# Kernel tuning notes

Measured on AMD Instinct MI355X. Metric: run time of the kernel, lower is better.

The kernel has to match this reference:

```python
import jax, jax.numpy as jnp
import numpy as np

NUM_EXPERTS = 8
TOP_K = 2
TOKENS = 4096
HIDDEN = 1024
INTER = 2048
INIT_STD = 0.01  # nnx.initializers.normal() default stddev


def setup_inputs() -> dict:
    key = jax.random.key(0)
    k1, k2, k3, k4, k5 = jax.random.split(key, 5)
    return {
        "inputs": jax.random.normal(k1, (TOKENS, HIDDEN), jnp.float32),
        "router_logits": jax.random.normal(k2, (TOKENS, NUM_EXPERTS), jnp.float32),
        "wi_0": jax.random.normal(k3, (NUM_EXPERTS, HIDDEN, INTER), jnp.float32) * INIT_STD,
        "wi_1": jax.random.normal(k4, (NUM_EXPERTS, HIDDEN, INTER), jnp.float32) * INIT_STD,
        "wo": jax.random.normal(k5, (NUM_EXPERTS, INTER, HIDDEN), jnp.float32) * INIT_STD,
    }


def reference(inputs, router_logits, wi_0, wi_1, wo):
    T, H = inputs.shape
    # --- top-k routing ---
    top_k_logits, top_k_indices = jax.lax.top_k(router_logits, TOP_K)  # [T, k]
    w = jax.nn.softmax(top_k_logits, axis=-1)
    w = w / jnp.sum(w, axis=-1, keepdims=True)  # (redundant renorm, kept faithful)
    # --- permute: sort token-expert pairs by expert id ---
    flat_experts = top_k_indices.reshape(-1)          # [T*k]
    sort_idx = jnp.argsort(flat_experts)              # stable sort -> token order within group
    token_idx = sort_idx // TOP_K                     # source token of each sorted slot
    x = inputs[token_idx]                             # [T*k, H] gathered/permuted tokens
    group_sizes = jnp.bincount(flat_experts, length=NUM_EXPERTS).astype(jnp.int32)
    # --- grouped (ragged) GEMM experts: silu(x@wi_0) * (x@wi_1) @ wo ---
    h0 = jax.lax.ragged_dot(x, wi_0, group_sizes, preferred_element_type=jnp.float32)
    h1 = jax.lax.ragged_dot(x, wi_1, group_sizes, preferred_element_type=jnp.float32)
    act = jax.nn.silu(h0) * h1                        # [T*k, INTER]
    y = jax.lax.ragged_dot(act, wo, group_sizes, preferred_element_type=jnp.float32)  # [T*k, H]
    # --- unpermute + weighted combine over top-k ---
    unsort = jnp.argsort(sort_idx)
    y = y[unsort].reshape(T, TOP_K, H)
    return jnp.sum(y * w[..., None], axis=1)          # [T, H]
```

## Files before the change

### kernel.cpp

```cpp
#include <hip/hip_runtime.h>
#include <hip/hip_bf16.h>

#define T_TOKENS 4096
#define HID 1024
#define INTER 2048
#define NEXP 8
#define TOPK 2
#define RTOT (T_TOKENS * TOPK)
#define BMT 128
#define BN 128
#define MAXT (RTOT / BMT + NEXP)

typedef __attribute__((ext_vector_type(8))) short bf16x8;
typedef __attribute__((ext_vector_type(4))) float f32x4;

typedef __attribute__((address_space(1))) const unsigned int gu32;
typedef __attribute__((address_space(3))) unsigned int lu32;

__device__ __forceinline__ void gl16(const void* g, void* l) {
  __builtin_amdgcn_global_load_lds((gu32*)g, (lu32*)l, 16, 0, 0);
}

__device__ __forceinline__ unsigned f2bf(float f) {
  union { float f; unsigned u; } v; v.f = f;
  unsigned u = v.u;
  return (u + 0x7FFFu + ((u >> 16) & 1u)) >> 16;
}

__device__ __forceinline__ float bf2f(unsigned short s) {
  union { unsigned u; float f; } v; v.u = ((unsigned)s) << 16;
  return v.f;
}

__device__ __forceinline__ int swz(int row, int kb) {
  return row * 128 + (kb ^ ((row & 7) << 4));
}

__device__ __forceinline__ void phase_barrier() {
  asm volatile("" ::: "memory");
  __builtin_amdgcn_s_barrier();
  asm volatile("" ::: "memory");
}

__device__ __forceinline__ int psig(int kap) { return kap ^ ((kap & 1) << 2); }

__global__ __launch_bounds__(1024)
void k_routing(const float* __restrict__ logits, int* ntiles,
               int* te2, int* tr02, int* tcnt2,
               float* pw, int* rows, float* rw, int* slotOf) {
  __shared__ int cnt[NEXP];
  __shared__ int cur[NEXP];
  const int tid = threadIdx.x;
  if (tid < NEXP) cnt[tid] = 0;
  __syncthreads();
#pragma unroll
  for (int j = 0; j < 4; ++j) {
    int t = j * 1024 + tid;
    float l[NEXP];
#pragma unroll
    for (int i = 0; i < NEXP; ++i) l[i] = logits[t * NEXP + i];
    int i0 = 0; float b0 = l[0];
#pragma unroll
    for (int i = 1; i < NEXP; ++i) if (l[i] > b0) { b0 = l[i]; i0 = i; }
    int i1 = -1; float b1 = -1e30f;
#pragma unroll
    for (int i = 0; i < NEXP; ++i) if (i != i0 && l[i] > b1) { b1 = l[i]; i1 = i; }
    float e = __expf(b1 - b0);
    float w0 = 1.f / (1.f + e);
    float w1 = e / (1.f + e);
    pw[2 * t] = w0; pw[2 * t + 1] = w1;
#pragma unroll
    for (int ex = 0; ex < NEXP; ++ex) {
      int c = __popcll(__ballot(i0 == ex)) + __popcll(__ballot(i1 == ex));
      if ((tid & 63) == 0 && c) atomicAdd(&cnt[ex], c);
    }
  }
  __syncthreads();
  if (tid == 0) {
    int off = 0, nm = 0;
    for (int e = 0; e < NEXP; ++e) {
      int c = cnt[e];
      cur[e] = off;
      for (int m0 = 0; m0 < c; m0 += BMT) {
        te2[nm] = e; tr02[nm] = off + m0; tcnt2[nm] = min(BMT, c - m0); ++nm;
      }
      off += c;
    }
    ntiles[1] = nm;
  }
  __syncthreads();
#pragma unroll
  for (int j = 0; j < 4; ++j) {
    int t = j * 1024 + tid;
    float l[NEXP];
#pragma unroll
    for (int i = 0; i < NEXP; ++i) l[i] = logits[t * NEXP + i];
    int i0 = 0; float b0 = l[0];
#pragma unroll
    for (int i = 1; i < NEXP; ++i) if (l[i] > b0) { b0 = l[i]; i0 = i; }
    int i1 = -1; float b1 = -1e30f;
#pragma unroll
    for (int i = 0; i < NEXP; ++i) if (i != i0 && l[i] > b1) { b1 = l[i]; i1 = i; }
    float e = __expf(b1 - b0);
    float ww[2] = {1.f / (1.f + e), e / (1.f + e)};
    int ee[2] = {i0, i1};
#pragma unroll
    for (int k = 0; k < TOPK; ++k) {
      int s = atomicAdd(&cur[ee[k]], 1);
      rows[s] = t;
      rw[s] = ww[k];
      slotOf[2 * t + k] = s;
    }
  }
}

__global__ __launch_bounds__(256)
void k_prep1r(const float* __restrict__ X, unsigned short* __restrict__ Xb,
              const float* __restrict__ W0, const float* __restrict__ W1,
              unsigned short* __restrict__ T0, unsigned short* __restrict__ T1,
              const float* __restrict__ logits, int* ntiles,
              int* te2, int* tr02, int* tcnt2,
              float* pw, int* rows, float* rw, int* slotOf) {
  int bid = blockIdx.x;
  const int tid = threadIdx.x;

  if (bid == 0) {
    __shared__ int cnt[NEXP];
    __shared__ int cur[NEXP];
    if (tid < NEXP) cnt[tid] = 0;
    __syncthreads();
#pragma unroll
    for (int j = 0; j < 16; ++j) {
      int t = j * 256 + tid;
      float l[NEXP];
#pragma unroll
      for (int i = 0; i < NEXP; ++i) l[i] = logits[t * NEXP + i];
      int i0 = 0; float b0 = l[0];
#pragma unroll
      for (int i = 1; i < NEXP; ++i) if (l[i] > b0) { b0 = l[i]; i0 = i; }
      int i1 = -1; float b1 = -1e30f;
#pragma unroll
      for (int i = 0; i < NEXP; ++i) if (i != i0 && l[i] > b1) { b1 = l[i]; i1 = i; }
      float e = __expf(b1 - b0);
      float w0 = 1.f / (1.f + e);
      pw[2 * t] = w0; pw[2 * t + 1] = 1.f - w0;
#pragma unroll
      for (int ex = 0; ex < NEXP; ++ex) {
        int c = __popcll(__ballot(i0 == ex)) + __popcll(__ballot(i1 == ex));
        if ((tid & 63) == 0 && c) atomicAdd(&cnt[ex], c);
      }
    }
    __syncthreads();
    if (tid == 0) {
      int off = 0, nm = 0;
      for (int e = 0; e < NEXP; ++e) {
        int c = cnt[e];
        cur[e] = off;
        for (int m0 = 0; m0 < c; m0 += BMT) {
          te2[nm] = e; tr02[nm] = off + m0; tcnt2[nm] = min(BMT, c - m0); ++nm;
        }
        off += c;
      }
      ntiles[1] = nm;
    }
    __syncthreads();
#pragma unroll
    for (int j = 0; j < 16; ++j) {
      int t = j * 256 + tid;
      float l[NEXP];
#pragma unroll
      for (int i = 0; i < NEXP; ++i) l[i] = logits[t * NEXP + i];
      int i0 = 0; float b0 = l[0];
#pragma unroll
      for (int i = 1; i < NEXP; ++i) if (l[i] > b0) { b0 = l[i]; i0 = i; }
      int i1 = -1; float b1 = -1e30f;
#pragma unroll
      for (int i = 0; i < NEXP; ++i) if (i != i0 && l[i] > b1) { b1 = l[i]; i1 = i; }
      float e = __expf(b1 - b0);
      float ww0 = 1.f / (1.f + e);
      int ee[2] = {i0, i1};
      float ww[2] = {ww0, 1.f - ww0};
#pragma unroll
      for (int k = 0; k < TOPK; ++k) {
        int s = atomicAdd(&cur[ee[k]], 1);
        rows[s] = t;
        rw[s] = ww[k];
        slotOf[2 * t + k] = s;
      }
    }
    return;
  }

  if (bid < 1025) {
    int base = (bid - 1) * 1024 + tid;
#pragma unroll
    for (int j = 0; j < 4; ++j) {
      int i = base + j * 256;
      float4 v = *(const float4*)(X + (size_t)i * 4);
      uint2 p;
      p.x = f2bf(v.x) | (f2bf(v.y) << 16);
      p.y = f2bf(v.z) | (f2bf(v.w) << 16);
      *(uint2*)(Xb + (size_t)i * 4) = p;
    }
    return;
  }
  bid -= 1025;
  const int w = bid >> 11;
  const int r = bid & 2047;
  const float* W = (w == 0) ? W0 : W1;
  unsigned short* T = (w == 0) ? T0 : T1;
  const int nt = r & 15, kt = (r >> 4) & 15, e = r >> 8;
  __shared__ float ls[64 * 128];
  const float* src = W + (size_t)e * HID * INTER + (size_t)(kt * 64) * INTER + nt * 128;
#pragma unroll
  for (int t = 0; t < 8; ++t) {
    int u = t * 256 + tid;
    int k = u >> 5, n4 = u & 31;
    float4 v = *(const float4*)(src + (size_t)k * INTER + n4 * 4);
    *(float4*)(ls + k * 128 + ((n4 ^ psig(k >> 3)) << 2)) = v;
  }
  __syncthreads();
  unsigned short* dst = T + (((size_t)e * 16 + nt) * 16 + kt) * 8192;
#pragma unroll
  for (int t = 0; t < 4; ++t) {
    int v = t * 256 + tid;
    int kt2 = v >> 9, n = (v >> 2) & 127, sw = v & 3;
    int kc = kt2 * 4 + (sw ^ ((n >> 1) & 3));
    const float* col = ls + (size_t)(kc * 8) * 128 +
                       (((n >> 2) ^ psig(kc)) << 2) + (n & 3);
    unsigned b[8];
#pragma unroll
    for (int i = 0; i < 8; ++i) b[i] = f2bf(col[i * 128]);
    uint4 q;
    q.x = b[0] | (b[1] << 16); q.y = b[2] | (b[3] << 16);
    q.z = b[4] | (b[5] << 16); q.w = b[6] | (b[7] << 16);
    *(uint4*)(dst + (size_t)v * 8) = q;
  }
}

__global__ __launch_bounds__(512, 4)
void k_gemm1w(const unsigned short* __restrict__ Xb,
              const unsigned short* __restrict__ WT0,
              const unsigned short* __restrict__ WT1,
              const float* __restrict__ WO,
              unsigned short* __restrict__ WTo,
              const int* __restrict__ ntiles, const int* __restrict__ te2,
              const int* __restrict__ tr02, const int* __restrict__ tcnt2,
              const int* __restrict__ rows,
              unsigned short* __restrict__ act) {
  const int ty = blockIdx.y;
  const int nt = blockIdx.x;
  const int tid = threadIdx.x;
  __shared__ __align__(16) unsigned char sm[49152];

  if (ty >= MAXT) {
    const int r = (ty - MAXT) * 16 + nt;
    const int ntt = r & 7, kt = (r >> 3) & 31, e = r >> 8;
    float* ls = (float*)sm;
    const float* src = WO + (size_t)e * INTER * HID + (size_t)(kt * 64) * HID + ntt * 128;
#pragma unroll
    for (int t = 0; t < 4; ++t) {
      int u = t * 512 + tid;
      int k = u >> 5, n4 = u & 31;
      float4 v = *(const float4*)(src + (size_t)k * HID + n4 * 4);
      *(float4*)(ls + k * 128 + ((n4 ^ psig(k >> 3)) << 2)) = v;
    }
    __syncthreads();
    unsigned short* dst = WTo + (((size_t)e * 8 + ntt) * 32 + kt) * 8192;
#pragma unroll
    for (int t = 0; t < 2; ++t) {
      int v = t * 512 + tid;
      int kt2 = v >> 9, n = (v >> 2) & 127, sw = v & 3;
      int kc = kt2 * 4 + (sw ^ ((n >> 1) & 3));
      const float* col = ls + (size_t)(kc * 8) * 128 +
                         (((n >> 2) ^ psig(kc)) << 2) + (n & 3);
      unsigned b[8];
#pragma unroll
      for (int i = 0; i < 8; ++i) b[i] = f2bf(col[i * 128]);
      uint4 q;
      q.x = b[0] | (b[1] << 16); q.y = b[2] | (b[3] << 16);
      q.z = b[4] | (b[5] << 16); q.w = b[6] | (b[7] << 16);
      *(uint4*)(dst + (size_t)v * 8) = q;
    }
    return;
  }

  if (ty >= ntiles[1]) return;
  const int e = te2[ty], row0 = tr02[ty], mcnt = tcnt2[ty];
  const int n0 = nt * BN;
  const int lane = tid & 63, wv = tid >> 6;
  const int mh = wv >> 2, nq = wv & 3;
  const int l15 = lane & 15, sl = lane >> 4;

  const int am = tid >> 2;
  const int atok = rows[row0 + (am < mcnt ? am : mcnt - 1)];
  const int askc = ((tid & 3) ^ ((tid >> 3) & 3)) * 8;
  const unsigned short* B0t = WT0 + ((size_t)e * 16 + nt) * 32 * 4096;
  const unsigned short* B1t = WT1 + ((size_t)e * 16 + nt) * 32 * 4096;

  int aoff[4], boff[2];
#pragma unroll
  for (int f = 0; f < 4; ++f) {
    int m = mh * 64 + f * 16 + l15;
    aoff[f] = m * 64 + ((sl ^ ((m >> 1) & 3)) << 4);
  }
#pragma unroll
  for (int g = 0; g < 2; ++g) {
    int n = nq * 32 + g * 16 + l15;
    boff[g] = n * 64 + ((sl ^ ((n >> 1) & 3)) << 4);
  }

  f32x4 acc0[4][2], acc1[4][2];
  const f32x4 zz = {0.f, 0.f, 0.f, 0.f};
#pragma unroll
  for (int f = 0; f < 4; ++f)
#pragma unroll
    for (int g = 0; g < 2; ++g) { acc0[f][g] = zz; acc1[f][g] = zz; }

  const int NT_K = HID / 32;

  gl16(Xb + (size_t)atok * HID + askc, sm + tid * 16);
  gl16(B0t + (size_t)tid * 8, sm + 8192 + tid * 16);
  gl16(B1t + (size_t)tid * 8, sm + 16384 + tid * 16);

  for (int t = 0; t < NT_K; ++t) {
    unsigned char* cur = sm + (t & 1) * 24576;
    unsigned char* nxt = sm + ((t + 1) & 1) * 24576;
    const int tn = (t + 1 < NT_K) ? (t + 1) : (NT_K - 1);

    gl16(Xb + (size_t)atok * HID + tn * 32 + askc, nxt + tid * 16);
    gl16(B0t + (size_t)tn * 4096 + tid * 8, nxt + 8192 + tid * 16);
    gl16(B1t + (size_t)tn * 4096 + tid * 8, nxt + 16384 + tid * 16);
    asm volatile("s_waitcnt vmcnt(3)" ::: "memory");
    __builtin_amdgcn_sched_barrier(0);
    phase_barrier();

    bf16x8 aA[4], b0q[2], b1q[2];
#pragma unroll
    for (int g = 0; g < 2; ++g) {
      b0q[g] = *(const bf16x8*)(cur + 8192 + boff[g]);
      b1q[g] = *(const bf16x8*)(cur + 16384 + boff[g]);
    }
#pragma unroll
    for (int f = 0; f < 4; ++f) aA[f] = *(const bf16x8*)(cur + aoff[f]);
    __builtin_amdgcn_s_setprio(1);
#pragma unroll
    for (int f = 0; f < 4; ++f)
#pragma unroll
      for (int g = 0; g < 2; ++g) {
        acc0[f][g] = __builtin_amdgcn_mfma_f32_16x16x32_bf16(aA[f], b0q[g], acc0[f][g], 0, 0, 0);
        acc1[f][g] = __builtin_amdgcn_mfma_f32_16x16x32_bf16(aA[f], b1q[g], acc1[f][g], 0, 0, 0);
      }
    __builtin_amdgcn_s_setprio(0);
    phase_barrier();
  }

#pragma unroll
  for (int f = 0; f < 4; ++f) {
#pragma unroll
    for (int r = 0; r < 4; ++r) {
      int m = mh * 64 + f * 16 + sl * 4 + r;
      if (m >= mcnt) continue;
      size_t base = (size_t)(row0 + m) * INTER + n0 + nq * 32 + l15;
#pragma unroll
      for (int g = 0; g < 2; ++g) {
        float h0 = acc0[f][g][r];
        float h1 = acc1[f][g][r];
        float s = h0 / (1.f + __expf(-h0));
        act[base + g * 16] = (unsigned short)f2bf(s * h1);
      }
    }
  }
}

__global__ __launch_bounds__(256, 4)
void k_gemm2n(const unsigned short* __restrict__ act,
              const unsigned short* __restrict__ WTo,
              const int* __restrict__ ntiles, const int* __restrict__ te2,
              const int* __restrict__ tr02, const int* __restrict__ tcnt2,
              unsigned short* __restrict__ y) {
  const int ty = blockIdx.y;
  if (ty >= ntiles[1]) return;
  const int e = te2[ty], row0 = tr02[ty], mcnt = tcnt2[ty];
  const int nt = blockIdx.x, n0 = nt * BN;
  const int tid = threadIdx.x, lane = tid & 63, wv = tid >> 6;
  const int wr = wv >> 1, wc = wv & 1;
  const int l15 = lane & 15, sl = lane >> 4;

  __shared__ __align__(16) unsigned char sm[32768];

  const int am0 = tid >> 2, am1 = 64 + (tid >> 2);
  const int ar0 = row0 + (am0 < mcnt ? am0 : mcnt - 1);
  const int ar1 = row0 + (am1 < mcnt ? am1 : mcnt - 1);
  const int askc = ((tid & 3) ^ ((tid >> 3) & 3)) * 8;
  const unsigned short* Bt = WTo + ((size_t)e * 8 + nt) * 64 * 4096;

  int aoff[4], boff[4];
#pragma unroll
  for (int f = 0; f < 4; ++f) {
    int m = wr * 64 + f * 16 + l15;
    aoff[f] = m * 64 + ((sl ^ ((m >> 1) & 3)) << 4);
    int n = wc * 64 + f * 16 + l15;
    boff[f] = n * 64 + ((sl ^ ((n >> 1) & 3)) << 4);
  }

  f32x4 acc[4][4];
  const f32x4 zz = {0.f, 0.f, 0.f, 0.f};
#pragma unroll
  for (int i = 0; i < 4; ++i)
#pragma unroll
    for (int j = 0; j < 4; ++j) acc[i][j] = zz;

  const int NT_K = INTER / 32;

  gl16(act + (size_t)ar0 * INTER + askc, sm + tid * 16);
  gl16(act + (size_t)ar1 * INTER + askc, sm + (256 + tid) * 16);
  gl16(Bt + (size_t)tid * 8, sm + 8192 + tid * 16);
  gl16(Bt + (size_t)(256 + tid) * 8, sm + 8192 + (256 + tid) * 16);

  for (int t = 0; t < NT_K; ++t) {
    unsigned char* cur = sm + (t & 1) * 16384;
    unsigned char* nxt = sm + ((t + 1) & 1) * 16384;
    const int tn = (t + 1 < NT_K) ? (t + 1) : (NT_K - 1);

    gl16(act + (size_t)ar0 * INTER + tn * 32 + askc, nxt + tid * 16);
    gl16(act + (size_t)ar1 * INTER + tn * 32 + askc, nxt + (256 + tid) * 16);
    gl16(Bt + (size_t)tn * 4096 + tid * 8, nxt + 8192 + tid * 16);
    gl16(Bt + ((size_t)tn * 4096 + 2048) + tid * 8, nxt + 8192 + (256 + tid) * 16);
    asm volatile("s_waitcnt vmcnt(4)" ::: "memory");
    __builtin_amdgcn_sched_barrier(0);
    phase_barrier();

    bf16x8 af[4], bb[4];
#pragma unroll
    for (int f = 0; f < 4; ++f) {
      af[f] = *(const bf16x8*)(cur + aoff[f]);
      bb[f] = *(const bf16x8*)(cur + 8192 + boff[f]);
    }
    __builtin_amdgcn_s_setprio(1);
#pragma unroll
    for (int mf = 0; mf < 4; ++mf)
#pragma unroll
      for (int nf = 0; nf < 4; ++nf)
        acc[mf][nf] = __builtin_amdgcn_mfma_f32_16x16x32_bf16(af[mf], bb[nf], acc[mf][nf], 0, 0, 0);
    __builtin_amdgcn_s_setprio(0);
    phase_barrier();
  }

#pragma unroll
  for (int mf = 0; mf < 4; ++mf) {
#pragma unroll
    for (int r = 0; r < 4; ++r) {
      int m = wr * 64 + mf * 16 + sl * 4 + r;
      if (m >= mcnt) continue;
      unsigned short* yp = y + (size_t)(row0 + m) * HID + n0 + wc * 64 + l15;
#pragma unroll
      for (int nf = 0; nf < 4; ++nf)
        yp[nf * 16] = (unsigned short)f2bf(acc[mf][nf][r]);
    }
  }
}

__global__ void k_combine(const unsigned short* __restrict__ y,
                          const float* __restrict__ pw,
                          const int* __restrict__ slotOf,
                          float* __restrict__ out) {
  int idx = blockIdx.x * blockDim.x + threadIdx.x;
  int t = idx >> 7, hc = (idx & 127) * 8;
  int s0 = slotOf[2 * t], s1 = slotOf[2 * t + 1];
  float w0 = pw[2 * t], w1 = pw[2 * t + 1];
  uint4 a = *(const uint4*)(y + (size_t)s0 * HID + hc);
  uint4 b = *(const uint4*)(y + (size_t)s1 * HID + hc);
  float o[8];
  const unsigned* ap = (const unsigned*)&a;
  const unsigned* bp = (const unsigned*)&b;
#pragma unroll
  for (int i = 0; i < 4; ++i) {
    o[2 * i]     = w0 * bf2f((unsigned short)(ap[i] & 0xFFFF)) + w1 * bf2f((unsigned short)(bp[i] & 0xFFFF));
    o[2 * i + 1] = w0 * bf2f((unsigned short)(ap[i] >> 16))    + w1 * bf2f((unsigned short)(bp[i] >> 16));
  }
  float* op = out + (size_t)t * HID + hc;
  *(float4*)op = make_float4(o[0], o[1], o[2], o[3]);
  *(float4*)(op + 4) = make_float4(o[4], o[5], o[6], o[7]);
}

__global__ __launch_bounds__(256, 2)
void k_gemm1_fb(const float* __restrict__ X, const float* __restrict__ W0,
                const float* __restrict__ W1, const int* __restrict__ ntiles,
                const int* __restrict__ te2, const int* __restrict__ tr02,
                const int* __restrict__ tcnt2, const int* __restrict__ rows,
                unsigned short* __restrict__ act) {
  const int ty = blockIdx.y;
  if (ty >= ntiles[1]) return;
  const int e = te2[ty], row0 = tr02[ty], mcnt = tcnt2[ty];
  const int n0 = blockIdx.x * BN;
  const int tid = threadIdx.x;
  const int lane = tid & 63, wv = tid >> 6;
  const int wr = wv >> 1, wc = wv & 1;

  __shared__ unsigned char smf[49152];
  unsigned char* As = smf;
  unsigned char* B0s = smf + 16384;
  unsigned char* B1s = smf + 32768;

  int atok[8];
#pragma unroll
  for (int j = 0; j < 8; ++j) {
    int m = (j * 256 + tid) >> 4;
    atok[j] = (m < mcnt) ? rows[row0 + m] : -1;
  }
  const int bnb = (tid & 7) | ((tid >> 7) << 6);
  const int bc = (tid >> 3) & 15;

  f32x4 acc0[4][4], acc1[4][4];
  const f32x4 zz = {0.f, 0.f, 0.f, 0.f};
#pragma unroll
  for (int i = 0; i < 4; ++i)
#pragma unroll
    for (int j = 0; j < 4; ++j) { acc0[i][j] = zz; acc1[i][j] = zz; }

  const float* W0e = W0 + (size_t)e * HID * INTER + n0;
  const float* W1e = W1 + (size_t)e * HID * INTER + n0;

  for (int k0 = 0; k0 < HID; k0 += 64) {
#pragma unroll
    for (int j = 0; j < 8; ++j) {
      int c = j * 256 + tid;
      int m = c >> 4, ch = c & 15;
      float4 v = make_float4(0.f, 0.f, 0.f, 0.f);
      int tok = atok[j];
      if (tok >= 0) v = *(const float4*)(X + (size_t)tok * HID + k0 + 4 * ch);
      uint2 p;
      p.x = f2bf(v.x) | (f2bf(v.y) << 16);
      p.y = f2bf(v.z) | (f2bf(v.w) << 16);
      *(uint2*)(As + swz(m, 8 * ch)) = p;
    }
#pragma unroll
    for (int j = 0; j < 8; ++j) {
      int n = bnb | (j << 3);
      const float* p0 = W0e + (size_t)(k0 + 4 * bc) * INTER + n;
      float a0 = p0[0], a1 = p0[INTER], a2 = p0[2 * INTER], a3 = p0[3 * INTER];
      uint2 q;
      q.x = f2bf(a0) | (f2bf(a1) << 16);
      q.y = f2bf(a2) | (f2bf(a3) << 16);
      *(uint2*)(B0s + swz(n, 8 * bc)) = q;
      const float* p1 = W1e + (size_t)(k0 + 4 * bc) * INTER + n;
      a0 = p1[0]; a1 = p1[INTER]; a2 = p1[2 * INTER]; a3 = p1[3 * INTER];
      q.x = f2bf(a0) | (f2bf(a1) << 16);
      q.y = f2bf(a2) | (f2bf(a3) << 16);
      *(uint2*)(B1s + swz(n, 8 * bc)) = q;
    }
    __syncthreads();
#pragma unroll
    for (int kq = 0; kq < 2; ++kq) {
      int kb = kq * 64 + 16 * (lane >> 4);
      bf16x8 a[4], b0[4], b1[4];
#pragma unroll
      for (int f = 0; f < 4; ++f) {
        int m = wr * 64 + f * 16 + (lane & 15);
        a[f] = *(const bf16x8*)(As + swz(m, kb));
        int n = wc * 64 + f * 16 + (lane & 15);
        b0[f] = *(const bf16x8*)(B0s + swz(n, kb));
        b1[f] = *(const bf16x8*)(B1s + swz(n, kb));
      }
#pragma unroll
      for (int mf = 0; mf < 4; ++mf)
#pragma unroll
        for (int nf = 0; nf < 4; ++nf) {
          acc0[mf][nf] = __builtin_amdgcn_mfma_f32_16x16x32_bf16(a[mf], b0[nf], acc0[mf][nf], 0, 0, 0);
          acc1[mf][nf] = __builtin_amdgcn_mfma_f32_16x16x32_bf16(a[mf], b1[nf], acc1[mf][nf], 0, 0, 0);
        }
    }
    __syncthreads();
  }
#pragma unroll
  for (int mf = 0; mf < 4; ++mf) {
#pragma unroll
    for (int r = 0; r < 4; ++r) {
      int m = wr * 64 + mf * 16 + (lane >> 4) * 4 + r;
      if (m >= mcnt) continue;
      size_t rowbase = (size_t)(row0 + m) * INTER + n0 + wc * 64 + (lane & 15);
#pragma unroll
      for (int nf = 0; nf < 4; ++nf) {
        float h0 = acc0[mf][nf][r];
        float h1 = acc1[mf][nf][r];
        float s = h0 / (1.f + __expf(-h0));
        act[rowbase + nf * 16] = (unsigned short)f2bf(s * h1);
      }
    }
  }
}

__global__ __launch_bounds__(256, 2)
void k_gemm2_fb(const unsigned short* __restrict__ act, const float* __restrict__ WO,
                const int* __restrict__ ntiles, const int* __restrict__ te2,
                const int* __restrict__ tr02, const int* __restrict__ tcnt2,
                const int* __restrict__ rows, const float* __restrict__ rw,
                float* __restrict__ out) {
  const int ty = blockIdx.y;
  if (ty >= ntiles[1]) return;
  const int e = te2[ty], row0 = tr02[ty], mcnt = tcnt2[ty];
  const int n0 = blockIdx.x * BN;
  const int tid = threadIdx.x;
  const int lane = tid & 63, wv = tid >> 6;
  const int wr = wv >> 1, wc = wv & 1;

  __shared__ unsigned char smf[32768];
  unsigned char* As = smf;
  unsigned char* Bs = smf + 16384;

  const int bnb = (tid & 7) | ((tid >> 7) << 6);
  const int bc = (tid >> 3) & 15;

  f32x4 acc[4][4];
  const f32x4 zz = {0.f, 0.f, 0.f, 0.f};
#pragma unroll
  for (int i = 0; i < 4; ++i)
#pragma unroll
    for (int j = 0; j < 4; ++j) acc[i][j] = zz;

  const float* We = WO + (size_t)e * INTER * HID + n0;

  for (int k0 = 0; k0 < INTER; k0 += 64) {
#pragma unroll
    for (int j = 0; j < 4; ++j) {
      int u = j * 256 + tid;
      int m = u >> 3, ch = u & 7;
      uint4 v = make_uint4(0u, 0u, 0u, 0u);
      if (m < mcnt)
        v = *(const uint4*)(act + (size_t)(row0 + m) * INTER + k0 + 8 * ch);
      *(uint4*)(As + swz(m, 16 * ch)) = v;
    }
#pragma unroll
    for (int j = 0; j < 8; ++j) {
      int n = bnb | (j << 3);
      const float* p = We + (size_t)(k0 + 4 * bc) * HID + n;
      float a0 = p[0], a1 = p[HID], a2 = p[2 * HID], a3 = p[3 * HID];
      uint2 q;
      q.x = f2bf(a0) | (f2bf(a1) << 16);
      q.y = f2bf(a2) | (f2bf(a3) << 16);
      *(uint2*)(Bs + swz(n, 8 * bc)) = q;
    }
    __syncthreads();
#pragma unroll
    for (int kq = 0; kq < 2; ++kq) {
      int kb = kq * 64 + 16 * (lane >> 4);
      bf16x8 a[4], b[4];
#pragma unroll
      for (int f = 0; f < 4; ++f) {
        int m = wr * 64 + f * 16 + (lane & 15);
        a[f] = *(const bf16x8*)(As + swz(m, kb));
        int n = wc * 64 + f * 16 + (lane & 15);
        b[f] = *(const bf16x8*)(Bs + swz(n, kb));
      }
#pragma unroll
      for (int mf = 0; mf < 4; ++mf)
#pragma unroll
        for (int nf = 0; nf < 4; ++nf)
          acc[mf][nf] = __builtin_amdgcn_mfma_f32_16x16x32_bf16(a[mf], b[nf], acc[mf][nf], 0, 0, 0);
    }
    __syncthreads();
  }
#pragma unroll
  for (int mf = 0; mf < 4; ++mf) {
#pragma unroll
    for (int r = 0; r < 4; ++r) {
      int m = wr * 64 + mf * 16 + (lane >> 4) * 4 + r;
      if (m >= mcnt) continue;
      int tok = rows[row0 + m];
      float w = rw[row0 + m];
      float* op = out + (size_t)tok * HID + n0 + wc * 64 + (lane & 15);
#pragma unroll
      for (int nf = 0; nf < 4; ++nf)
        atomicAdd(op + nf * 16, w * acc[mf][nf][r]);
    }
  }
}

extern "C" void kernel_launch(void* const* d_in, const int* in_sizes, int n_in,
                              void* d_out, int out_size, void* d_ws, size_t ws_size,
                              hipStream_t stream) {
  const float* X  = (const float*)d_in[0];
  const float* RL = (const float*)d_in[1];
  const float* W0 = (const float*)d_in[2];
  const float* W1 = (const float*)d_in[3];
  const float* WOp = (const float*)d_in[4];
  float* out = (float*)d_out;

  char* ws = (char*)d_ws;
  int* ntiles  = (int*)(ws + 128);
  int* te2     = (int*)(ws + 2048);
  int* tr02    = (int*)(ws + 2560);
  int* tcnt2   = (int*)(ws + 3072);
  float* pw    = (float*)(ws + 8192 + 32768);
  int* rows    = (int*)(ws + 8192 + 65536);
  float* rw    = (float*)(ws + 8192 + 98304);
  int* slotOf  = (int*)(ws + 8192 + 131072);

  const bool big = ws_size >= ((size_t)145 << 20);

  if (big) {
    unsigned short* Xb  = (unsigned short*)(ws + ((size_t)1 << 20));
    unsigned short* act = (unsigned short*)(ws + ((size_t)16 << 20));
    unsigned short* WT0 = (unsigned short*)(ws + ((size_t)48 << 20));
    unsigned short* WT1 = (unsigned short*)(ws + ((size_t)80 << 20));
    unsigned short* WTo = (unsigned short*)(ws + ((size_t)112 << 20));
    unsigned short* y   = (unsigned short*)(ws + ((size_t)48 << 20));

    k_prep1r<<<5121, 256, 0, stream>>>(X, Xb, W0, W1, WT0, WT1,
                                       RL, ntiles, te2, tr02, tcnt2,
                                       pw, rows, rw, slotOf);

    k_gemm1w<<<dim3(INTER / BN, MAXT + 128), 512, 0, stream>>>(
        Xb, WT0, WT1, WOp, WTo, ntiles, te2, tr02, tcnt2, rows, act);
    k_gemm2n<<<dim3(HID / BN, MAXT), 256, 0, stream>>>(act, WTo, ntiles, te2, tr02, tcnt2, y);
    k_combine<<<(T_TOKENS * HID / 8) / 256, 256, 0, stream>>>(y, pw, slotOf, out);
  } else {
    unsigned short* act = (unsigned short*)(ws + ((size_t)1 << 20));
    hipMemsetAsync(d_out, 0, (size_t)out_size * sizeof(float), stream);
    k_routing<<<1, 1024, 0, stream>>>(RL, ntiles, te2, tr02, tcnt2, pw, rows, rw, slotOf);
    k_gemm1_fb<<<dim3(INTER / BN, MAXT), 256, 0, stream>>>(X, W0, W1, ntiles, te2, tr02, tcnt2, rows, act);
    k_gemm2_fb<<<dim3(HID / BN, MAXT), 256, 0, stream>>>(act, WOp, ntiles, te2, tr02, tcnt2, rows, rw, out);
  }
}
```

Measured before the change: 211.5 us.

## Interleave WO transpose blocks with GEMM1 tiles and use packed bf16 convert

Replaces the manual round-to-nearest-even float-to-bf16 conversion with the hardware v_cvt_pk_bf16_f32 instruction in the input and weight conversion paths. It also reorders the blockIdx.y mapping of the GEMM1 launch so WO-transpose blocks alternate with GEMM tiles rather than all trailing at the end. The grid becomes 200 rows (72 GEMM rows interleaved with 72 WO rows, then 56 more WO rows). The goal is to overlap the bandwidth-bound transpose with compute-bound GEMM work and shrink the conversion instruction count. The hardware convert's rounding may differ slightly from the software version for NaN or edge cases.

Measured after the change: 237.2 us. 12.1% more time.

```diff
diff --git a/kernel.cpp b/kernel.cpp
--- a/kernel.cpp
+++ b/kernel.cpp
@@ -25,6 +25,12 @@
   union { float f; unsigned u; } v; v.f = f;
   unsigned u = v.u;
   return (u + 0x7FFFu + ((u >> 16) & 1u)) >> 16;
+}
+
+__device__ __forceinline__ unsigned cvtpk(float lo, float hi) {
+  unsigned r;
+  asm("v_cvt_pk_bf16_f32 %0, %1, %2" : "=v"(r) : "v"(lo), "v"(hi));
+  return r;
 }
 
 __device__ __forceinline__ float bf2f(unsigned short s) {
@@ -198,8 +204,8 @@
       int i = base + j * 256;
       float4 v = *(const float4*)(X + (size_t)i * 4);
       uint2 p;
-      p.x = f2bf(v.x) | (f2bf(v.y) << 16);
-      p.y = f2bf(v.z) | (f2bf(v.w) << 16);
+      p.x = cvtpk(v.x, v.y);
+      p.y = cvtpk(v.z, v.w);
       *(uint2*)(Xb + (size_t)i * 4) = p;
     }
     return;
@@ -228,12 +234,11 @@
     int kc = kt2 * 4 + (sw ^ ((n >> 1) & 3));
     const float* col = ls + (size_t)(kc * 8) * 128 +
                        (((n >> 2) ^ psig(kc)) << 2) + (n & 3);
-    unsigned b[8];
-#pragma unroll
-    for (int i = 0; i < 8; ++i) b[i] = f2bf(col[i * 128]);
     uint4 q;
-    q.x = b[0] | (b[1] << 16); q.y = b[2] | (b[3] << 16);
-    q.z = b[4] | (b[5] << 16); q.w = b[6] | (b[7] << 16);
+    q.x = cvtpk(col[0 * 128], col[1 * 128]);
+    q.y = cvtpk(col[2 * 128], col[3 * 128]);
+    q.z = cvtpk(col[4 * 128], col[5 * 128]);
+    q.w = cvtpk(col[6 * 128], col[7 * 128]);
     *(uint4*)(dst + (size_t)v * 8) = q;
   }
 }
@@ -248,13 +253,15 @@
               const int* __restrict__ tr02, const int* __restrict__ tcnt2,
               const int* __restrict__ rows,
               unsigned short* __restrict__ act) {
-  const int ty = blockIdx.y;
+  const int tyr = blockIdx.y;
   const int nt = blockIdx.x;
   const int tid = threadIdx.x;
   __shared__ __align__(16) unsigned char sm[49152];
 
-  if (ty >= MAXT) {
-    const int r = (ty - MAXT) * 16 + nt;
+  const bool isWO = (tyr < 144) ? ((tyr & 1) != 0) : true;
+  if (isWO) {
+    const int wq = (tyr < 144) ? (tyr >> 1) : (72 + (tyr - 144));
+    const int r = wq * 16 + nt;
     const int ntt = r & 7, kt = (r >> 3) & 31, e = r >> 8;
     float* ls = (float*)sm;
     const float* src = WO + (size_t)e * INTER * HID + (size_t)(kt * 64) * HID + ntt * 128;
@@ -274,17 +281,17 @@
       int kc = kt2 * 4 + (sw ^ ((n >> 1) & 3));
       const float* col = ls + (size_t)(kc * 8) * 128 +
                          (((n >> 2) ^ psig(kc)) << 2) + (n & 3);
-      unsigned b[8];
-#pragma unroll
-      for (int i = 0; i < 8; ++i) b[i] = f2bf(col[i * 128]);
       uint4 q;
-      q.x = b[0] | (b[1] << 16); q.y = b[2] | (b[3] << 16);
-      q.z = b[4] | (b[5] << 16); q.w = b[6] | (b[7] << 16);
+      q.x = cvtpk(col[0 * 128], col[1 * 128]);
+      q.y = cvtpk(col[2 * 128], col[3 * 128]);
+      q.z = cvtpk(col[4 * 128], col[5 * 128]);
+      q.w = cvtpk(col[6 * 128], col[7 * 128]);
       *(uint4*)(dst + (size_t)v * 8) = q;
     }
     return;
   }
 
+  const int ty = tyr >> 1;
   if (ty >= ntiles[1]) return;
   const int e = te2[ty], row0 = tr02[ty], mcnt = tcnt2[ty];
   const int n0 = nt * BN;
@@ -711,7 +718,7 @@
                                        RL, ntiles, te2, tr02, tcnt2,
                                        pw, rows, rw, slotOf);
 
-    k_gemm1w<<<dim3(INTER / BN, MAXT + 128), 512, 0, stream>>>(
+    k_gemm1w<<<dim3(INTER / BN, 200), 512, 0, stream>>>(
         Xb, WT0, WT1, WOp, WTo, ntiles, te2, tr02, tcnt2, rows, act);
     k_gemm2n<<<dim3(HID / BN, MAXT), 256, 0, stream>>>(act, WTo, ntiles, te2, tr02, tcnt2, y);
     k_combine<<<(T_TOKENS * HID / 8) / 256, 256, 0, stream>>>(y, pw, slotOf, out);
```
